# Performance work log

Hardware: AMD Instinct MI355X
Metric: run time of the kernel (lower is better)

## Reference

```python
import jax, jax.numpy as jnp
import numpy as np

B, S, D, H = 2, 2048, 1024, 16
DH = D // H  # depth per head = 64


def setup_inputs() -> dict:
    key = jax.random.key(0)
    ks = jax.random.split(key, 5)
    sc = 0.02
    return {
        "x": jax.random.normal(ks[0], (B, S, D), dtype=jnp.float32),
        "Wq": jax.random.normal(ks[1], (D, D), dtype=jnp.float32) * sc,
        "bq": jnp.zeros((D,), dtype=jnp.float32),
        "Wk": jax.random.normal(ks[2], (D, D), dtype=jnp.float32) * sc,
        "bk": jnp.zeros((D,), dtype=jnp.float32),
        "Wv": jax.random.normal(ks[3], (D, D), dtype=jnp.float32) * sc,
        "bv": jnp.zeros((D,), dtype=jnp.float32),
        "Wo": jax.random.normal(ks[4], (D, D), dtype=jnp.float32) * sc,
        "bo": jnp.zeros((D,), dtype=jnp.float32),
    }


def _split_heads(t):
    # [B,S,D] -> [B,H,S,DH]
    return t.reshape(B, S, H, DH).transpose(0, 2, 1, 3)


def reference(x, Wq, bq, Wk, bk, Wv, bv, Wo, bo):
    q = _split_heads(x @ Wq + bq)
    k = _split_heads(x @ Wk + bk)
    v = _split_heads(x @ Wv + bv)
    scale = 1.0 / jnp.sqrt(jnp.float32(DH))
    logits = jnp.einsum("bhqd,bhkd->bhqk", q, k) * scale  # [B,H,S,S]
    attn = jax.nn.softmax(logits, axis=-1)
    ctx = jnp.einsum("bhqk,bhkd->bhqd", attn, v)
    ctx = ctx.transpose(0, 2, 1, 3).reshape(B, S, D)
    # dropout is identity at inference
    return ctx @ Wo + bo
```

## Files before the change

### kernel.cpp

```cpp
#include <hip/hip_runtime.h>
#include <hip/hip_bf16.h>

#define S_LEN   2048
#define D_MODEL 1024
#define NHEAD   16
#define DHEAD   64
#define M_ROWS  4096
#define BHEADS  32

typedef __attribute__((ext_vector_type(8)))  short short8;
typedef __attribute__((ext_vector_type(4)))  float f32x4;
typedef __attribute__((ext_vector_type(16))) float f32x16;
typedef __attribute__((ext_vector_type(4)))  unsigned short us4;

extern "C" __device__ float __ocml_native_exp2_f32(float);

__device__ __forceinline__ unsigned short f2b(float f) {
    unsigned int u = __builtin_bit_cast(unsigned int, f);
    return (unsigned short)((u + 0x7FFFu + ((u >> 16) & 1u)) >> 16);
}

__device__ __forceinline__ unsigned int pk2b(float lo, float hi) {
    unsigned int u0 = __builtin_bit_cast(unsigned int, lo) + 0x8000u;
    unsigned int u1 = __builtin_bit_cast(unsigned int, hi) + 0x8000u;
    return __builtin_amdgcn_perm(u1, u0, 0x07060302u);
}

#define GLOAD16(gp, lp) __builtin_amdgcn_global_load_lds(                     \
        (const __attribute__((address_space(1))) void*)(gp),                  \
        (__attribute__((address_space(3))) void*)(lp), 16, 0, 0)

#define STAGE_OFS(lane) ((((lane) & 3) ^ (((lane) >> 3) & 3)) * 8)

__global__ __launch_bounds__(256) void prep(
    const float* __restrict__ x, unsigned short* __restrict__ xb,
    const float* __restrict__ Wq, const float* __restrict__ Wk,
    const float* __restrict__ Wv, const float* __restrict__ Wo,
    unsigned short* __restrict__ Wqt, unsigned short* __restrict__ Wkt,
    unsigned short* __restrict__ Wvt, unsigned short* __restrict__ Wot)
{
    const int z = blockIdx.z;
    const int tx = threadIdx.x, ty = threadIdx.y;
    if (z == 4) {
        const int blk = blockIdx.y * 32 + blockIdx.x;
        const int base = (blk * 256 + ty * 32 + tx) * 4;
        #pragma unroll
        for (int r = 0; r < 4; ++r) {
            const int i = base + r * (M_ROWS * D_MODEL / 4);
            const float4 v = *(const float4*)&x[i];
            us4 o;
            o.x = f2b(v.x); o.y = f2b(v.y); o.z = f2b(v.z); o.w = f2b(v.w);
            *(us4*)&xb[i] = o;
        }
        return;
    }
    __shared__ float tile[32][33];
    const float* W = z == 0 ? Wq : (z == 1 ? Wk : (z == 2 ? Wv : Wo));
    unsigned short* Wt = z == 0 ? Wqt : (z == 1 ? Wkt : (z == 2 ? Wvt : Wot));
    const int n0 = blockIdx.x * 32, k0 = blockIdx.y * 32;
    #pragma unroll
    for (int i = 0; i < 4; ++i)
        tile[ty + i * 8][tx] = W[(size_t)(k0 + ty + i * 8) * D_MODEL + n0 + tx];
    __syncthreads();
    #pragma unroll
    for (int i = 0; i < 4; ++i)
        Wt[(size_t)(n0 + ty + i * 8) * D_MODEL + k0 + tx] = f2b(tile[tx][ty + i * 8]);
}

__global__ __launch_bounds__(256) void gemm_qkv(
    const unsigned short* __restrict__ xb,
    const unsigned short* __restrict__ Wqt, const unsigned short* __restrict__ Wkt,
    const unsigned short* __restrict__ Wvt,
    const float* __restrict__ bq, const float* __restrict__ bk,
    const float* __restrict__ bv,
    unsigned short* __restrict__ Qb, unsigned short* __restrict__ Kb,
    unsigned short* __restrict__ Vt)
{
    __shared__ unsigned short As[2][128][32];
    __shared__ unsigned short Bs[2][128][32];

    const int z = blockIdx.z;
    const unsigned short* Wt = z == 0 ? Wqt : (z == 1 ? Wkt : Wvt);
    const float* bias = z == 0 ? bq : (z == 1 ? bk : bv);

    const int t = threadIdx.x, lane = t & 63, w = t >> 6;
    const int wm = w >> 1, wn = w & 1;
    const int bm = blockIdx.y * 128, bn = blockIdx.x * 128;
    const int lr = lane >> 2, lc = STAGE_OFS(lane);
    const int lm = lane & 15, quad = lane >> 4;
    const int qo = (quad ^ ((lm >> 1) & 3)) * 8;

    f32x4 acc[4][4] = {};

    #pragma unroll
    for (int i = 0; i < 2; ++i) {
        const int c = 2 * w + i;
        GLOAD16(xb + (size_t)(bm + c * 16 + lr) * D_MODEL + lc, &As[0][c * 16][0]);
        GLOAD16(Wt + (size_t)(bn + c * 16 + lr) * D_MODEL + lc, &Bs[0][c * 16][0]);
    }
    __syncthreads();

    for (int it = 0; it < 32; ++it) {
        const int cur = it & 1;
        if (it + 1 < 32) {
            const int kt = (it + 1) * 32;
            #pragma unroll
            for (int i = 0; i < 2; ++i) {
                const int c = 2 * w + i;
                GLOAD16(xb + (size_t)(bm + c * 16 + lr) * D_MODEL + kt + lc,
                        &As[cur ^ 1][c * 16][0]);
                GLOAD16(Wt + (size_t)(bn + c * 16 + lr) * D_MODEL + kt + lc,
                        &Bs[cur ^ 1][c * 16][0]);
            }
        }

        short8 af[4], bfr[4];
        #pragma unroll
        for (int mi = 0; mi < 4; ++mi)
            af[mi] = *(const short8*)&As[cur][wm * 64 + mi * 16 + lm][qo];
        #pragma unroll
        for (int ni = 0; ni < 4; ++ni)
            bfr[ni] = *(const short8*)&Bs[cur][wn * 64 + ni * 16 + lm][qo];
        #pragma unroll
        for (int mi = 0; mi < 4; ++mi)
            #pragma unroll
            for (int ni = 0; ni < 4; ++ni)
                acc[mi][ni] = __builtin_amdgcn_mfma_f32_16x16x32_bf16(
                    af[mi], bfr[ni], acc[mi][ni], 0, 0, 0);

        __syncthreads();
    }

    float bb[4];
    #pragma unroll
    for (int ni = 0; ni < 4; ++ni)
        bb[ni] = bias[bn + wn * 64 + ni * 16 + lm];
    const float scale = (z == 0) ? 0.18033688011112042f : 1.0f;

    if (z < 2) {
        unsigned short* Out = (z == 0) ? Qb : Kb;
        #pragma unroll
        for (int mi = 0; mi < 4; ++mi)
            #pragma unroll
            for (int r = 0; r < 4; ++r) {
                const int row = bm + wm * 64 + mi * 16 + quad * 4 + r;
                const int b = row >> 11, s = row & 2047;
                #pragma unroll
                for (int ni = 0; ni < 4; ++ni) {
                    const int col = bn + wn * 64 + ni * 16 + lm;
                    const int h = col >> 6, d = col & 63;
                    Out[(((size_t)(b * NHEAD + h)) * S_LEN + s) * DHEAD + d] =
                        f2b((acc[mi][ni][r] + bb[ni]) * scale);
                }
            }
    } else {
        #pragma unroll
        for (int mi = 0; mi < 4; ++mi) {
            const int row0 = bm + wm * 64 + mi * 16 + quad * 4;
            const int b = row0 >> 11, s0 = row0 & 2047;
            #pragma unroll
            for (int ni = 0; ni < 4; ++ni) {
                const int col = bn + wn * 64 + ni * 16 + lm;
                const int h = col >> 6, d = col & 63;
                us4 pk;
                pk.x = f2b(acc[mi][ni][0] + bb[ni]);
                pk.y = f2b(acc[mi][ni][1] + bb[ni]);
                pk.z = f2b(acc[mi][ni][2] + bb[ni]);
                pk.w = f2b(acc[mi][ni][3] + bb[ni]);
                *(us4*)&Vt[(((size_t)(b * NHEAD + h)) * DHEAD + d) * S_LEN + s0] = pk;
            }
        }
    }
}

__global__ __launch_bounds__(256) void gemm_out(
    const unsigned short* __restrict__ Ab, const unsigned short* __restrict__ Wot,
    const float* __restrict__ bo, float* __restrict__ out)
{
    __shared__ unsigned short As[2][64][32];
    __shared__ unsigned short Bs[2][128][32];

    const int t = threadIdx.x, lane = t & 63, w = t >> 6;
    const int wm = w & 1, wn = w >> 1;
    const int bm = blockIdx.y * 64, bn = blockIdx.x * 128;
    const int lr = lane >> 2, lc = STAGE_OFS(lane);
    const int lm = lane & 15, quad = lane >> 4;
    const int qo = (quad ^ ((lm >> 1) & 3)) * 8;

    f32x4 acc[2][4] = {};

    GLOAD16(Ab + (size_t)(bm + w * 16 + lr) * D_MODEL + lc, &As[0][w * 16][0]);
    #pragma unroll
    for (int i = 0; i < 2; ++i)
        GLOAD16(Wot + (size_t)(bn + w * 32 + i * 16 + lr) * D_MODEL + lc,
                &Bs[0][w * 32 + i * 16][0]);
    __syncthreads();

    for (int it = 0; it < 32; ++it) {
        const int cur = it & 1;
        if (it + 1 < 32) {
            const int kt = (it + 1) * 32;
            GLOAD16(Ab + (size_t)(bm + w * 16 + lr) * D_MODEL + kt + lc,
                    &As[cur ^ 1][w * 16][0]);
            #pragma unroll
            for (int i = 0; i < 2; ++i)
                GLOAD16(Wot + (size_t)(bn + w * 32 + i * 16 + lr) * D_MODEL + kt + lc,
                        &Bs[cur ^ 1][w * 32 + i * 16][0]);
        }

        short8 af[2], bfr[4];
        #pragma unroll
        for (int mi = 0; mi < 2; ++mi)
            af[mi] = *(const short8*)&As[cur][wm * 32 + mi * 16 + lm][qo];
        #pragma unroll
        for (int ni = 0; ni < 4; ++ni)
            bfr[ni] = *(const short8*)&Bs[cur][wn * 64 + ni * 16 + lm][qo];
        #pragma unroll
        for (int mi = 0; mi < 2; ++mi)
            #pragma unroll
            for (int ni = 0; ni < 4; ++ni)
                acc[mi][ni] = __builtin_amdgcn_mfma_f32_16x16x32_bf16(
                    af[mi], bfr[ni], acc[mi][ni], 0, 0, 0);

        __syncthreads();
    }

    float bb[4];
    #pragma unroll
    for (int ni = 0; ni < 4; ++ni)
        bb[ni] = bo[bn + wn * 64 + ni * 16 + lm];

    #pragma unroll
    for (int mi = 0; mi < 2; ++mi)
        #pragma unroll
        for (int r = 0; r < 4; ++r) {
            const int row = bm + wm * 32 + mi * 16 + quad * 4 + r;
            #pragma unroll
            for (int ni = 0; ni < 4; ++ni) {
                const int col = bn + wn * 64 + ni * 16 + lm;
                out[(size_t)row * D_MODEL + col] = acc[mi][ni][r] + bb[ni];
            }
        }
}

__global__ __launch_bounds__(256) void attn_mfma(
    const unsigned short* __restrict__ Q, const unsigned short* __restrict__ K,
    const unsigned short* __restrict__ V, unsigned short* __restrict__ Cx)
{
    __shared__ unsigned short Qs[2][128][32];
    __shared__ unsigned short Ks[2][2][64][32];
    __shared__ unsigned short Vs[2][2][64][32];
    __shared__ unsigned int   Ps[4][32][36];

    const int t = threadIdx.x, lane = t & 63, w = t >> 6;
    const int q5 = lane & 31, hi = lane >> 5;
    const int lr = lane >> 2, lcs = STAGE_OFS(lane);
    const int q0 = blockIdx.x * 128, bh = blockIdx.y;
    const int sw = (q5 >> 1) & 3;
    int sbo[4];
    #pragma unroll
    for (int sb = 0; sb < 4; ++sb) sbo[sb] = (sb ^ sw) * 8;

    const unsigned short* Qh = Q + (size_t)bh * (S_LEN * DHEAD);
    const unsigned short* Kh = K + (size_t)bh * (S_LEN * DHEAD);
    const unsigned short* Vh = V + (size_t)bh * (DHEAD * S_LEN);

    #pragma unroll
    for (int i = 0; i < 2; ++i)
        #pragma unroll
        for (int c = 0; c < 2; ++c)
            GLOAD16(Qh + (size_t)(q0 + w * 32 + c * 16 + lr) * DHEAD + i * 32 + lcs,
                    &Qs[i][w * 32 + c * 16][0]);
    #pragma unroll
    for (int i = 0; i < 2; ++i) {
        GLOAD16(Kh + (size_t)(w * 16 + lr) * DHEAD + i * 32 + lcs, &Ks[0][i][w * 16][0]);
        GLOAD16(Vh + (size_t)(w * 16 + lr) * S_LEN + i * 32 + lcs, &Vs[0][i][w * 16][0]);
    }
    __syncthreads();

    short8 qf[4];
    #pragma unroll
    for (int c = 0; c < 4; ++c)
        qf[c] = *(const short8*)&Qs[c >> 1][w * 32 + q5][sbo[(c & 1) * 2 + hi]];

    f32x16 acc[2] = {};
    float2 l2a = {0.f, 0.f}, l2b = {0.f, 0.f};

    for (int it = 0; it < 32; ++it) {
        const int cur = it & 1;
        if (it + 1 < 32) {
            const int kt = (it + 1) * 64;
            #pragma unroll
            for (int i = 0; i < 2; ++i) {
                GLOAD16(Kh + (size_t)(kt + w * 16 + lr) * DHEAD + i * 32 + lcs,
                        &Ks[cur ^ 1][i][w * 16][0]);
                GLOAD16(Vh + (size_t)(w * 16 + lr) * S_LEN + kt + i * 32 + lcs,
                        &Vs[cur ^ 1][i][w * 16][0]);
            }
        }

        f32x16 sf[2] = {};
        #pragma unroll
        for (int c = 0; c < 4; ++c) {
            #pragma unroll
            for (int mt = 0; mt < 2; ++mt) {
                const short8 kf =
                    *(const short8*)&Ks[cur][c >> 1][mt * 32 + q5][sbo[(c & 1) * 2 + hi]];
                sf[mt] = __builtin_amdgcn_mfma_f32_32x32x16_bf16(kf, qf[c], sf[mt], 0, 0, 0);
            }
        }

        #pragma unroll
        for (int mt = 0; mt < 2; ++mt)
            #pragma unroll
            for (int g = 0; g < 4; ++g) {
                const float p0 = __ocml_native_exp2_f32(sf[mt][g * 4 + 0]);
                const float p1 = __ocml_native_exp2_f32(sf[mt][g * 4 + 1]);
                const float p2 = __ocml_native_exp2_f32(sf[mt][g * 4 + 2]);
                const float p3 = __ocml_native_exp2_f32(sf[mt][g * 4 + 3]);
                l2a.x += p0; l2a.y += p1;
                l2b.x += p2; l2b.y += p3;
                uint2 pk;
                pk.x = pk2b(p0, p1);
                pk.y = pk2b(p2, p3);
                *(uint2*)&Ps[w][q5][mt * 16 + g * 4 + hi * 2] = pk;
            }

        #pragma unroll
        for (int c = 0; c < 4; ++c) {
            const short8 pf = *(const short8*)&Ps[w][q5][c * 8 + hi * 4];
            #pragma unroll
            for (int nt = 0; nt < 2; ++nt) {
                const short8 vf =
                    *(const short8*)&Vs[cur][c >> 1][nt * 32 + q5][sbo[(c & 1) * 2 + hi]];
                acc[nt] = __builtin_amdgcn_mfma_f32_32x32x16_bf16(pf, vf, acc[nt], 0, 0, 0);
            }
        }

        __syncthreads();
    }

    float l_acc = (l2a.x + l2a.y) + (l2b.x + l2b.y);
    l_acc += __shfl_xor(l_acc, 32);
    const float inv = 1.f / l_acc;
    const int b = bh >> 4, h = bh & 15;
    #pragma unroll
    for (int reg = 0; reg < 16; ++reg) {
        const int row = (reg & 3) + 8 * (reg >> 2) + 4 * hi;
        const float invr = __shfl(inv, row);
        const int s = q0 + w * 32 + row;
        const size_t base = ((size_t)(b * S_LEN + s)) * D_MODEL + h * DHEAD;
        Cx[base + q5]      = f2b(acc[0][reg] * invr);
        Cx[base + 32 + q5] = f2b(acc[1][reg] * invr);
    }
}

extern "C" void kernel_launch(void* const* d_in, const int* in_sizes, int n_in,
                              void* d_out, int out_size, void* d_ws, size_t ws_size,
                              hipStream_t stream)
{
    const float* x  = (const float*)d_in[0];
    const float* Wq = (const float*)d_in[1];
    const float* bq = (const float*)d_in[2];
    const float* Wk = (const float*)d_in[3];
    const float* bk = (const float*)d_in[4];
    const float* Wv = (const float*)d_in[5];
    const float* bv = (const float*)d_in[6];
    const float* Wo = (const float*)d_in[7];
    const float* bo = (const float*)d_in[8];
    float* out = (float*)d_out;

    unsigned short* xb  = (unsigned short*)d_ws;
    unsigned short* Wqt = xb  + (size_t)M_ROWS * D_MODEL;
    unsigned short* Wkt = Wqt + (size_t)D_MODEL * D_MODEL;
    unsigned short* Wvt = Wkt + (size_t)D_MODEL * D_MODEL;
    unsigned short* Wot = Wvt + (size_t)D_MODEL * D_MODEL;
    unsigned short* Qb  = Wot + (size_t)D_MODEL * D_MODEL;
    unsigned short* Kb  = Qb  + (size_t)M_ROWS * D_MODEL;
    unsigned short* Vt  = Kb  + (size_t)M_ROWS * D_MODEL;
    unsigned short* Cxb = Vt  + (size_t)M_ROWS * D_MODEL;

    prep<<<dim3(32, 32, 5), dim3(32, 8), 0, stream>>>(
        x, xb, Wq, Wk, Wv, Wo, Wqt, Wkt, Wvt, Wot);

    gemm_qkv<<<dim3(D_MODEL / 128, M_ROWS / 128, 3), dim3(256), 0, stream>>>(
        xb, Wqt, Wkt, Wvt, bq, bk, bv, Qb, Kb, Vt);

    attn_mfma<<<dim3(S_LEN / 128, BHEADS), dim3(256), 0, stream>>>(Qb, Kb, Vt, Cxb);

    gemm_out<<<dim3(D_MODEL / 128, M_ROWS / 64), dim3(256), 0, stream>>>(
        Cxb, Wot, bo, out);
}
```

Baseline: 210.5 us.

## Split attention over key dimension with partial outputs and reduction kernel

Splits the attention kernel into two key-range halves (split-K/flash-decoding style), doubling the grid from 512 to 1024 blocks, and adds an attn_reduce kernel that sums the bf16 partial outputs and normalizes by the combined softmax denominators. It drops the K/V double buffering in favor of single buffers with two barriers per iteration, aliases Q and P shared memory, and sets launch bounds for 4 blocks per CU to raise occupancy. The workspace is relaid out so the partial outputs reuse the xb buffer. The intent is better CU utilization. The costs are an extra kernel launch, extra global traffic for the partials, lost load/compute overlap, and partials rounded to bf16 before summation.

```diff
diff --git a/kernel.cpp b/kernel.cpp
--- a/kernel.cpp
+++ b/kernel.cpp
@@ -7,6 +7,7 @@
 #define DHEAD   64
 #define M_ROWS  4096
 #define BHEADS  32
+#define MEG     1048576
 
 typedef __attribute__((ext_vector_type(8)))  short short8;
 typedef __attribute__((ext_vector_type(4)))  float f32x4;
@@ -24,6 +25,10 @@
     unsigned int u0 = __builtin_bit_cast(unsigned int, lo) + 0x8000u;
     unsigned int u1 = __builtin_bit_cast(unsigned int, hi) + 0x8000u;
     return __builtin_amdgcn_perm(u1, u0, 0x07060302u);
+}
+
+__device__ __forceinline__ float b2f(unsigned short b) {
+    return __builtin_bit_cast(float, (unsigned int)b << 16);
 }
 
 #define GLOAD16(gp, lp) __builtin_amdgcn_global_load_lds(                     \
@@ -243,19 +248,22 @@
         }
 }
 
-__global__ __launch_bounds__(256) void attn_mfma(
+__global__ __launch_bounds__(256, 4) void attn_mfma(
     const unsigned short* __restrict__ Q, const unsigned short* __restrict__ K,
-    const unsigned short* __restrict__ V, unsigned short* __restrict__ Cx)
-{
-    __shared__ unsigned short Qs[2][128][32];
-    __shared__ unsigned short Ks[2][2][64][32];
-    __shared__ unsigned short Vs[2][2][64][32];
-    __shared__ unsigned int   Ps[4][32][36];
+    const unsigned short* __restrict__ V,
+    unsigned short* __restrict__ Opart, float* __restrict__ Lpart)
+{
+    __shared__ __align__(16) unsigned char QPraw[18432];
+    unsigned short (*Qs)[128][32] = (unsigned short (*)[128][32])QPraw;
+    unsigned int   (*Ps)[32][36]  = (unsigned int   (*)[32][36])QPraw;
+    __shared__ unsigned short Ks[2][64][32];
+    __shared__ unsigned short Vs[2][64][32];
 
     const int t = threadIdx.x, lane = t & 63, w = t >> 6;
     const int q5 = lane & 31, hi = lane >> 5;
     const int lr = lane >> 2, lcs = STAGE_OFS(lane);
-    const int q0 = blockIdx.x * 128, bh = blockIdx.y;
+    const int q0 = blockIdx.x * 128, bh = blockIdx.y, split = blockIdx.z;
+    const int k_base = split * (S_LEN / 2);
     const int sw = (q5 >> 1) & 3;
     int sbo[4];
     #pragma unroll
@@ -271,11 +279,6 @@
         for (int c = 0; c < 2; ++c)
             GLOAD16(Qh + (size_t)(q0 + w * 32 + c * 16 + lr) * DHEAD + i * 32 + lcs,
                     &Qs[i][w * 32 + c * 16][0]);
-    #pragma unroll
-    for (int i = 0; i < 2; ++i) {
-        GLOAD16(Kh + (size_t)(w * 16 + lr) * DHEAD + i * 32 + lcs, &Ks[0][i][w * 16][0]);
-        GLOAD16(Vh + (size_t)(w * 16 + lr) * S_LEN + i * 32 + lcs, &Vs[0][i][w * 16][0]);
-    }
     __syncthreads();
 
     short8 qf[4];
@@ -286,18 +289,17 @@
     f32x16 acc[2] = {};
     float2 l2a = {0.f, 0.f}, l2b = {0.f, 0.f};
 
-    for (int it = 0; it < 32; ++it) {
-        const int cur = it & 1;
-        if (it + 1 < 32) {
-            const int kt = (it + 1) * 64;
-            #pragma unroll
-            for (int i = 0; i < 2; ++i) {
-                GLOAD16(Kh + (size_t)(kt + w * 16 + lr) * DHEAD + i * 32 + lcs,
-                        &Ks[cur ^ 1][i][w * 16][0]);
-                GLOAD16(Vh + (size_t)(w * 16 + lr) * S_LEN + kt + i * 32 + lcs,
-                        &Vs[cur ^ 1][i][w * 16][0]);
-            }
-        }
+    for (int it = 0; it < 16; ++it) {
+        const int kt = k_base + it * 64;
+        __syncthreads();
+        #pragma unroll
+        for (int i = 0; i < 2; ++i) {
+            GLOAD16(Kh + (size_t)(kt + w * 16 + lr) * DHEAD + i * 32 + lcs,
+                    &Ks[i][w * 16][0]);
+            GLOAD16(Vh + (size_t)(w * 16 + lr) * S_LEN + kt + i * 32 + lcs,
+                    &Vs[i][w * 16][0]);
+        }
+        __syncthreads();
 
         f32x16 sf[2] = {};
         #pragma unroll
@@ -305,7 +307,7 @@
             #pragma unroll
             for (int mt = 0; mt < 2; ++mt) {
                 const short8 kf =
-                    *(const short8*)&Ks[cur][c >> 1][mt * 32 + q5][sbo[(c & 1) * 2 + hi]];
+                    *(const short8*)&Ks[c >> 1][mt * 32 + q5][sbo[(c & 1) * 2 + hi]];
                 sf[mt] = __builtin_amdgcn_mfma_f32_32x32x16_bf16(kf, qf[c], sf[mt], 0, 0, 0);
             }
         }
@@ -332,27 +334,47 @@
             #pragma unroll
             for (int nt = 0; nt < 2; ++nt) {
                 const short8 vf =
-                    *(const short8*)&Vs[cur][c >> 1][nt * 32 + q5][sbo[(c & 1) * 2 + hi]];
+                    *(const short8*)&Vs[c >> 1][nt * 32 + q5][sbo[(c & 1) * 2 + hi]];
                 acc[nt] = __builtin_amdgcn_mfma_f32_32x32x16_bf16(pf, vf, acc[nt], 0, 0, 0);
             }
         }
-
-        __syncthreads();
     }
 
     float l_acc = (l2a.x + l2a.y) + (l2b.x + l2b.y);
     l_acc += __shfl_xor(l_acc, 32);
-    const float inv = 1.f / l_acc;
-    const int b = bh >> 4, h = bh & 15;
+    const size_t pbase = ((size_t)(split * BHEADS + bh)) * S_LEN;
+    if (hi == 0)
+        Lpart[pbase + q0 + w * 32 + q5] = l_acc;
     #pragma unroll
     for (int reg = 0; reg < 16; ++reg) {
         const int row = (reg & 3) + 8 * (reg >> 2) + 4 * hi;
-        const float invr = __shfl(inv, row);
-        const int s = q0 + w * 32 + row;
-        const size_t base = ((size_t)(b * S_LEN + s)) * D_MODEL + h * DHEAD;
-        Cx[base + q5]      = f2b(acc[0][reg] * invr);
-        Cx[base + 32 + q5] = f2b(acc[1][reg] * invr);
-    }
+        const size_t obase = (pbase + q0 + w * 32 + row) * DHEAD;
+        Opart[obase + q5]      = f2b(acc[0][reg]);
+        Opart[obase + 32 + q5] = f2b(acc[1][reg]);
+    }
+}
+
+__global__ __launch_bounds__(256) void attn_reduce(
+    const unsigned short* __restrict__ Op, const float* __restrict__ Lp,
+    unsigned short* __restrict__ Cx)
+{
+    const int idx = blockIdx.x * 256 + threadIdx.x;
+    const int gi = idx * 4;
+    const int bh = gi >> 17;
+    const int rem = gi & (S_LEN * DHEAD - 1);
+    const int s = rem >> 6, d = rem & 63;
+    const size_t o0 = (size_t)bh * (S_LEN * DHEAD) + rem;
+    const size_t o1 = o0 + (size_t)BHEADS * S_LEN * DHEAD;
+    const us4 a = *(const us4*)&Op[o0];
+    const us4 c = *(const us4*)&Op[o1];
+    const float inv = 1.f / (Lp[bh * S_LEN + s] + Lp[BHEADS * S_LEN + bh * S_LEN + s]);
+    us4 o;
+    o.x = f2b((b2f(a.x) + b2f(c.x)) * inv);
+    o.y = f2b((b2f(a.y) + b2f(c.y)) * inv);
+    o.z = f2b((b2f(a.z) + b2f(c.z)) * inv);
+    o.w = f2b((b2f(a.w) + b2f(c.w)) * inv);
+    const int b = bh >> 4, h = bh & 15;
+    *(us4*)&Cx[((size_t)(b * S_LEN + s)) * D_MODEL + h * DHEAD + d] = o;
 }
 
 extern "C" void kernel_launch(void* const* d_in, const int* in_sizes, int n_in,
@@ -370,15 +392,18 @@
     const float* bo = (const float*)d_in[8];
     float* out = (float*)d_out;
 
-    unsigned short* xb  = (unsigned short*)d_ws;
-    unsigned short* Wqt = xb  + (size_t)M_ROWS * D_MODEL;
-    unsigned short* Wkt = Wqt + (size_t)D_MODEL * D_MODEL;
-    unsigned short* Wvt = Wkt + (size_t)D_MODEL * D_MODEL;
-    unsigned short* Wot = Wvt + (size_t)D_MODEL * D_MODEL;
-    unsigned short* Qb  = Wot + (size_t)D_MODEL * D_MODEL;
-    unsigned short* Kb  = Qb  + (size_t)M_ROWS * D_MODEL;
-    unsigned short* Vt  = Kb  + (size_t)M_ROWS * D_MODEL;
-    unsigned short* Cxb = Vt  + (size_t)M_ROWS * D_MODEL;
+    unsigned short* base = (unsigned short*)d_ws;
+    unsigned short* Wot   = base;
+    unsigned short* Qb    = base + 1 * MEG;
+    unsigned short* Kb    = base + 5 * MEG;
+    unsigned short* Vt    = base + 9 * MEG;
+    unsigned short* Cxb   = base + 13 * MEG;
+    unsigned short* xb    = base + 17 * MEG;
+    unsigned short* Wqt   = base + 21 * MEG;
+    unsigned short* Wkt   = base + 22 * MEG;
+    unsigned short* Wvt   = base + 23 * MEG;
+    unsigned short* Opart = xb;
+    float*          Lpart = (float*)(base + 25 * MEG);
 
     prep<<<dim3(32, 32, 5), dim3(32, 8), 0, stream>>>(
         x, xb, Wq, Wk, Wv, Wo, Wqt, Wkt, Wvt, Wot);
@@ -386,7 +411,11 @@
     gemm_qkv<<<dim3(D_MODEL / 128, M_ROWS / 128, 3), dim3(256), 0, stream>>>(
         xb, Wqt, Wkt, Wvt, bq, bk, bv, Qb, Kb, Vt);
 
-    attn_mfma<<<dim3(S_LEN / 128, BHEADS), dim3(256), 0, stream>>>(Qb, Kb, Vt, Cxb);
+    attn_mfma<<<dim3(S_LEN / 128, BHEADS, 2), dim3(256), 0, stream>>>(
+        Qb, Kb, Vt, Opart, Lpart);
+
+    attn_reduce<<<dim3(BHEADS * S_LEN * DHEAD / 1024), dim3(256), 0, stream>>>(
+        Opart, Lpart, Cxb);
 
     gemm_out<<<dim3(D_MODEL / 128, M_ROWS / 64), dim3(256), 0, stream>>>(
         Cxb, Wot, bo, out);
```

Measured after the change: 205.8 us. 2.2% less time.
